# Performance work log

Hardware: AMD Instinct MI355X
Metric: run time of the kernel (lower is better)

Reference implementation:

```python
import jax, jax.numpy as jnp
import numpy as np

K = 8
B = 3.0
DIM = 32
HID = 32
BATCH = 65536
MIN_BW = 1e-3
MIN_BH = 1e-3
MIN_D = 1e-3


def setup_inputs() -> dict:
    key = jax.random.key(0)
    ks = jax.random.split(key, 8)
    L = DIM - 1
    x = jax.random.normal(ks[0], (BATCH, DIM), jnp.float32)
    init_param = jax.random.uniform(ks[1], (3 * K - 1,), jnp.float32, -0.5, 0.5)
    # stacked per-dim FCNN weights; layer l conditions on x[:, :l+1] -> causal zero-mask
    w1 = jax.random.normal(ks[2], (L, L, HID), jnp.float32) * 0.2
    mask = (jnp.arange(L)[None, :] <= jnp.arange(L)[:, None]).astype(jnp.float32)
    w1 = w1 * mask[:, :, None]
    b1 = jax.random.normal(ks[3], (L, HID), jnp.float32) * 0.1
    w2 = jax.random.normal(ks[4], (L, HID, HID), jnp.float32) * 0.2
    b2 = jax.random.normal(ks[5], (L, HID), jnp.float32) * 0.1
    w3 = jax.random.normal(ks[6], (L, HID, 3 * K - 1), jnp.float32) * 0.2
    b3 = jax.random.normal(ks[7], (L, 3 * K - 1), jnp.float32) * 0.1
    return {"x": x, "init_param": init_param, "w1": w1, "b1": b1,
            "w2": w2, "b2": b2, "w3": w3, "b3": b3}


def _rqs_forward(x, Wu, Hu, Du):
    # x: [dim, batch]; Wu, Hu: [dim, batch, K]; Du: [dim, batch, K-1]
    inside = (x >= -B) & (x <= B)
    xc = jnp.clip(x, -B, B)
    # bin widths
    widths = jax.nn.softmax(Wu, axis=-1)
    widths = MIN_BW + (1.0 - MIN_BW * K) * widths
    cw = jnp.cumsum(widths, axis=-1)
    cw = jnp.concatenate([jnp.zeros(cw.shape[:-1] + (1,), cw.dtype), cw], axis=-1)
    cw = 2.0 * B * cw - B
    cw = cw.at[..., 0].set(-B).at[..., -1].set(B)
    widths = cw[..., 1:] - cw[..., :-1]
    # bin heights
    heights = jax.nn.softmax(Hu, axis=-1)
    heights = MIN_BH + (1.0 - MIN_BH * K) * heights
    ch = jnp.cumsum(heights, axis=-1)
    ch = jnp.concatenate([jnp.zeros(ch.shape[:-1] + (1,), ch.dtype), ch], axis=-1)
    ch = 2.0 * B * ch - B
    ch = ch.at[..., 0].set(-B).at[..., -1].set(B)
    heights = ch[..., 1:] - ch[..., :-1]
    # knot derivatives, edges pinned so softplus(const)+min_d = 1
    const = float(np.log(np.exp(1.0 - MIN_D) - 1.0))
    pad = jnp.full(Du.shape[:-1] + (1,), const, Du.dtype)
    derivs = MIN_D + jax.nn.softplus(jnp.concatenate([pad, Du, pad], axis=-1))  # [.., K+1]
    # bin search (searchsorted on cumwidths, eps bump on last edge)
    cw_s = cw.at[..., -1].add(1e-6)
    idx = jnp.sum((xc[..., None] >= cw_s).astype(jnp.int32), axis=-1) - 1
    idx = jnp.clip(idx, 0, K - 1)
    g = lambda a: jnp.take_along_axis(a, idx[..., None], axis=-1)[..., 0]
    in_cw = g(cw)
    in_w = g(widths)
    in_ch = g(ch)
    in_h = g(heights)
    in_delta = g(heights / widths)
    d0 = g(derivs)
    d1 = g(derivs[..., 1:])
    theta = (xc - in_cw) / in_w
    tt = theta * (1.0 - theta)
    num = in_h * (in_delta * theta ** 2 + d0 * tt)
    den = in_delta + (d0 + d1 - 2.0 * in_delta) * tt
    out = in_ch + num / den
    dnum = in_delta ** 2 * (d1 * theta ** 2 + 2.0 * in_delta * tt + d0 * (1.0 - theta) ** 2)
    ld = jnp.log(dnum) - 2.0 * jnp.log(den)
    out = jnp.where(inside, out, x)  # identity tails
    ld = jnp.where(inside, ld, 0.0)
    return out, ld


def reference(x, init_param, w1, b1, w2, b2, w3, b3):
    # all per-dim conditioners at once (w1 is causally masked in setup)
    h1 = jnp.tanh(jnp.einsum('bd,ldh->lbh', x[:, :DIM - 1], w1) + b1[:, None, :])
    h2 = jnp.tanh(jnp.einsum('lbh,lhg->lbg', h1, w2) + b2[:, None, :])
    out = jnp.einsum('lbh,lho->lbo', h2, w3) + b3[:, None, :]  # [dim-1, batch, 3K-1]
    p0 = jnp.broadcast_to(init_param, (1, x.shape[0], 3 * K - 1))
    params = jnp.concatenate([p0, out], axis=0)  # [dim, batch, 3K-1]
    Wu = 2.0 * B * jax.nn.softmax(params[..., :K], axis=-1)
    Hu = 2.0 * B * jax.nn.softmax(params[..., K:2 * K], axis=-1)
    Du = jax.nn.softplus(params[..., 2 * K:])
    z_t, ld = _rqs_forward(x.T, Wu, Hu, Du)  # [dim, batch]
    return z_t.T, jnp.sum(ld, axis=0)
```

## Files before the change

kernel.cpp:

```cpp
#include <hip/hip_runtime.h>
#include <hip/hip_bf16.h>
#include <cmath>

constexpr int KN   = 8;
constexpr int NPAR = 23;
constexpr int DD   = 32;
constexpr float BND   = 3.0f;
constexpr float MINBW = 1e-3f;
constexpr float MIND  = 1e-3f;

#define TPB   64
#define ROWS  64
#define GDIMS 4
#define WST   40
#define PSTH  28
#define RECB  8192

typedef __attribute__((ext_vector_type(8))) short short8;
typedef __attribute__((ext_vector_type(4))) float float4v;
typedef __attribute__((ext_vector_type(2))) __fp16 fp16x2;
typedef __attribute__((ext_vector_type(4))) _Float16 half4v;

#define RCP(x) __builtin_amdgcn_rcpf(x)

#if __has_builtin(__builtin_amdgcn_exp2f)
#define EXP2(x) __builtin_amdgcn_exp2f(x)
#else
#define EXP2(x) __expf((x) * 0.6931471805599453f)
#endif
#if __has_builtin(__builtin_amdgcn_logf)
#define LOG2F(x) __builtin_amdgcn_logf(x)
#else
#define LOG2F(x) __log2f(x)
#endif
#define MED3(x, lo, hi) __builtin_amdgcn_fmed3f((x), (lo), (hi))

constexpr float L2E = 1.4426950408889634f;
constexpr float LN2 = 0.6931471805599453f;

__device__ __forceinline__ short f2bf(float f) {
    unsigned u = __float_as_uint(f);
    u += 0x7fffu + ((u >> 16) & 1u);
    return (short)(u >> 16);
}

__device__ __forceinline__ int pkbf(float a, float b) {
    union { __hip_bfloat162 v; int i; } u;
    u.v = __float22bfloat162_rn(make_float2(a, b));
    return u.i;
}

__device__ __forceinline__ int pkh(float a, float b) {
    union { fp16x2 h; int i; } u;
    u.h = __builtin_amdgcn_cvt_pkrtz(a, b);
    return u.i;
}

__device__ __forceinline__ float4v tanh4v(float4v c) {
    constexpr float C2L = 2.0f * L2E;
    float e0 = EXP2(MED3(c[0], -10.f, 10.f) * C2L);
    float e1 = EXP2(MED3(c[1], -10.f, 10.f) * C2L);
    float e2 = EXP2(MED3(c[2], -10.f, 10.f) * C2L);
    float e3 = EXP2(MED3(c[3], -10.f, 10.f) * C2L);
    float a0 = e0 + 1.f, a1 = e1 + 1.f, a2 = e2 + 1.f, a3 = e3 + 1.f;
    float p01 = a0 * a1, p23 = a2 * a3;
    float r   = RCP(p01 * p23);
    float r01 = r * p23;
    float r23 = r * p01;
    float4v o;
    o[0] = fmaf(-2.f, r01 * a1, 1.f);
    o[1] = fmaf(-2.f, r01 * a0, 1.f);
    o[2] = fmaf(-2.f, r23 * a3, 1.f);
    o[3] = fmaf(-2.f, r23 * a2, 1.f);
    return o;
}

__device__ __forceinline__ float rqs_apply(float xv, const float* p, float& ldout) {
    constexpr float C1 = 2.0f * BND * MINBW;
    constexpr float FC = 2.0f * BND * (1.0f - MINBW * KN);

    float t0w[KN], t0h[KN];
#pragma unroll
    for (int k = 0; k < KN; ++k) t0w[k] = EXP2(p[k]);
#pragma unroll
    for (int k = 0; k < KN; ++k) t0h[k] = EXP2(p[KN + k]);
    float sw = ((t0w[0] + t0w[1]) + (t0w[2] + t0w[3]))
             + ((t0w[4] + t0w[5]) + (t0w[6] + t0w[7]));
    float sh = ((t0h[0] + t0h[1]) + (t0h[2] + t0h[3]))
             + ((t0h[4] + t0h[5]) + (t0h[6] + t0h[7]));
    float r1   = RCP(sw * sh);
    float invw = (2.0f * BND * L2E) * (r1 * sh);
    float invh = (2.0f * BND * L2E) * (r1 * sw);
    float e2w[KN], e2h[KN];
#pragma unroll
    for (int k = 0; k < KN; ++k) e2w[k] = EXP2(t0w[k] * invw);
#pragma unroll
    for (int k = 0; k < KN; ++k) e2h[k] = EXP2(t0h[k] * invh);
    float s2w = ((e2w[0] + e2w[1]) + (e2w[2] + e2w[3]))
              + ((e2w[4] + e2w[5]) + (e2w[6] + e2w[7]));
    float s2h = ((e2h[0] + e2h[1]) + (e2h[2] + e2h[3]))
              + ((e2h[4] + e2h[5]) + (e2h[6] + e2h[7]));
    float r2   = RCP(s2w * s2h);
    float facw = FC * (r2 * s2h);
    float fach = FC * (r2 * s2w);

    float xc = MED3(xv, -BND, BND);

    float w0 = fmaf(facw, e2w[0], C1);
    float h0 = fmaf(fach, e2h[0], C1);
    float in_cw = -BND, in_w = w0, in_ch = -BND, in_h = h0;
    float dl0 = 0.0f, dl1 = p[2 * KN];
    bool e0 = true, e1 = false;
    float cwk = -BND + w0;
    float chk = -BND + h0;
#pragma unroll
    for (int k = 1; k < KN; ++k) {
        float wk = fmaf(facw, e2w[k], C1);
        float hk = fmaf(fach, e2h[k], C1);
        bool c = (xc >= cwk);
        in_cw = c ? cwk : in_cw;
        in_w  = c ? wk  : in_w;
        in_ch = c ? chk : in_ch;
        in_h  = c ? hk  : in_h;
        dl0   = c ? p[2 * KN + k - 1] : dl0;
        if (k < KN - 1) dl1 = c ? p[2 * KN + k] : dl1;
        if (k == 1)      e0 = !c;
        if (k == KN - 1) e1 = c;
        cwk += wk;
        chk += hk;
    }
    in_w = e1 ? (BND - in_cw) : in_w;
    in_h = e1 ? (BND - in_ch) : in_h;

    float sp0 = LOG2F(2.0f + EXP2(dl0));
    float sp1 = LOG2F(2.0f + EXP2(dl1));
    float d0 = e0 ? 1.0f : fmaf(LN2, sp0, MIND);
    float d1 = e1 ? 1.0f : fmaf(LN2, sp1, MIND);

    float u  = xc - in_cw;
    float v  = in_w - u;
    float s  = in_w, h = in_h;
    float uu = u * u, vv = v * v, uv = u * v;
    float uvs = uv * s;
    float t   = fmaf(v, v, uu);
    float dd  = d0 + d1;
    float DEN = fmaf(h, t, dd * uvs);
    float rD  = RCP(DEN);
    float NUM = fmaf(h, uu, d0 * uvs);
    float z   = fmaf(h * NUM, rD, in_ch);
    float t2  = fmaf(d0, vv, d1 * uu);
    float DN  = fmaf(h + h, uv, t2 * s);
    float h2s = (h * h) * s;
    float larg = ((h2s * DN) * rD) * rD;

    bool inside = (xv >= -BND) && (xv <= BND);
    ldout = inside ? LN2 * LOG2F(larg) : 0.0f;
    return inside ? z : xv;
}

__device__ __forceinline__ short8 xpose_h(float4v cA, float4v cB,
                                          int odd, int sl_a, int sl_b, bool qlow) {
    float4v tA = tanh4v(cA);
    float4v tB = tanh4v(cB);
    int a0 = pkbf(tA[0], tA[1]);
    int a1 = pkbf(tA[2], tA[3]);
    int b0 = pkbf(tB[0], tB[1]);
    int b1 = pkbf(tB[2], tB[3]);
    int p0 = odd ? b0 : a0, p1 = odd ? b1 : a1;
    int p2 = odd ? a0 : b0, p3 = odd ? a1 : b1;
    int g0 = __shfl(p0, sl_a, 64);
    int g1 = __shfl(p1, sl_a, 64);
    int g2 = __shfl(p2, sl_b, 64);
    int g3 = __shfl(p3, sl_b, 64);
    union { int4 i; short8 s; } u;
    u.i = qlow ? make_int4(g0, g1, g2, g3) : make_int4(g2, g3, g0, g1);
    return u.s;
}

__device__ __forceinline__ float4v f4v(float4 v) {
    float4v r; r[0] = v.x; r[1] = v.y; r[2] = v.z; r[3] = v.w; return r;
}

struct WFrag {
    short8 w1a, w1b, w2a, w2b, w3a, w3b;
    float4v bA1, bB1, bA2, bB2, bA3, bB3;
};

__device__ __forceinline__ WFrag load_wfrag(const char* __restrict__ wbuf,
                                            int l, int ln, int q) {
    const char* rec = wbuf + (size_t)l * RECB;
    const short* rw = (const short*)rec;
    const float* rb = (const float*)(rec + 7680);
    WFrag f;
    f.w1a = *(const short8*)&rw[ln * WST + q * 8];
    f.w1b = *(const short8*)&rw[(16 + ln) * WST + q * 8];
    f.w2a = *(const short8*)&rw[1280 + ln * WST + q * 8];
    f.w2b = *(const short8*)&rw[1280 + (16 + ln) * WST + q * 8];
    f.w3a = *(const short8*)&rw[2560 + ln * WST + q * 8];
    f.w3b = *(const short8*)&rw[2560 + (16 + ln) * WST + q * 8];
    f.bA1 = f4v(*(const float4*)&rb[4 * q]);
    f.bB1 = f4v(*(const float4*)&rb[16 + 4 * q]);
    f.bA2 = f4v(*(const float4*)&rb[32 + 4 * q]);
    f.bB2 = f4v(*(const float4*)&rb[48 + 4 * q]);
    f.bA3 = f4v(*(const float4*)&rb[64 + 4 * q]);
    f.bB3 = f4v(*(const float4*)&rb[80 + 4 * q]);
    return f;
}

extern "C" __global__ void __launch_bounds__(256)
k_prep(const float* __restrict__ w1, const float* __restrict__ b1,
       const float* __restrict__ w2, const float* __restrict__ b2,
       const float* __restrict__ w3, const float* __restrict__ b3,
       char* __restrict__ wbuf, float* __restrict__ ldo, int B)
{
    const int l = blockIdx.x, tid = threadIdx.x;
    if (l >= 31) {
        const int zb = l - 31;
        const int chunk = B >> 6;
        float4* dst = (float4*)(ldo + (size_t)zb * chunk);
        for (int i = tid; i < (chunk >> 2); i += 256)
            dst[i] = make_float4(0.f, 0.f, 0.f, 0.f);
        return;
    }
    short* r1 = (short*)(wbuf + (size_t)l * RECB);
    short* r2 = r1 + 1280;
    short* r3 = r2 + 1280;
    float* f1 = (float*)(wbuf + (size_t)l * RECB + 7680);
    float* f2 = f1 + 32;
    float* f3 = f2 + 32;
    const float* g1 = w1 + (size_t)l * 992;
    const float* g2 = w2 + (size_t)l * 1024;
    const float* g3 = w3 + (size_t)l * 736;
    for (int i = tid; i < 1280; i += 256) {
        int n = i / WST, k = i - WST * n;
        r1[i] = (k < 31) ? f2bf(g1[k * 32 + n]) : (short)0;
        r2[i] = (k < 32) ? f2bf(g2[k * 32 + n]) : (short)0;
        r3[i] = (n < 23 && k < 32) ? f2bf(g3[k * 23 + n] * L2E) : (short)0;
    }
    if (tid < 32) { f1[tid] = b1[(size_t)l * 32 + tid]; f2[tid] = b2[(size_t)l * 32 + tid]; }
    if (tid < 32) f3[tid] = (tid < 23) ? b3[(size_t)l * 23 + tid] * L2E : 0.0f;
}

extern "C" __global__ void __launch_bounds__(TPB, 2)
k_nsf(const float* __restrict__ x,
      const float* __restrict__ p0,
      const char* __restrict__ wbuf,
      float* __restrict__ zo, float* __restrict__ ldo, int B)
{
    __shared__ __align__(16) _Float16 sP[ROWS * PSTH];

    const int tid  = threadIdx.x;
    const int lane = tid & 63;
    const int q    = lane >> 4;
    const int ln   = lane & 15;
    const int qb   = q & 1;
    const bool qlow = (q < 2);
    const int s_even = ln + 32 * qb;
    const int s_odd  = s_even + 16;
    const int sl_a = qlow ? s_even : s_odd;
    const int sl_b = qlow ? s_odd  : s_even;
    const int g    = blockIdx.y;
    const int ly0  = GDIMS * g;
    const long long rowbase = (long long)blockIdx.x * ROWS;
    const long long row = rowbase + tid;

    float xarr[GDIMS];
    {
        float4 xs = *(const float4*)(x + row * DD + ly0);
        xarr[0] = xs.x; xarr[1] = xs.y; xarr[2] = xs.z; xarr[3] = xs.w;
    }

    short8 au[4];
#pragma unroll
    for (int t = 0; t < 4; ++t) {
        const int m0 = 16 * t;
        const float4* xp = (const float4*)(x + (rowbase + m0 + ln) * DD + q * 8);
        float4 uu = xp[0], vv = xp[1];
        union { int4 i; short8 s; } c;
        c.i = make_int4(pkbf(uu.x, uu.y), pkbf(uu.z, uu.w),
                        pkbf(vv.x, vv.y), pkbf(vv.z, vv.w));
        au[t] = c.s;
    }

    float zreg[GDIMS];
    float ldacc = 0.0f;

    WFrag wf = load_wfrag(wbuf, (ly0 == 0) ? 0 : ly0 - 1, ln, q);

#pragma unroll
    for (int j = 0; j < GDIMS; ++j) {
        const int ly = ly0 + j;
        if (ly == 0) {
            float pr[NPAR];
#pragma unroll
            for (int k = 0; k < NPAR; ++k) pr[k] = p0[k] * L2E;
            float ld;
            zreg[0] = rqs_apply(xarr[0], pr, ld);
            ldacc += ld;
            continue;
        }

        float4v cA[4], cB[4];
#pragma unroll
        for (int t = 0; t < 4; ++t) {
            cA[t] = __builtin_amdgcn_mfma_f32_16x16x32_bf16(wf.w1a, au[t], wf.bA1, 0, 0, 0);
            cB[t] = __builtin_amdgcn_mfma_f32_16x16x32_bf16(wf.w1b, au[t], wf.bB1, 0, 0, 0);
        }
        short8 h1f[4];
#pragma unroll
        for (int t = 0; t < 4; ++t)
            h1f[t] = xpose_h(cA[t], cB[t], qb, sl_a, sl_b, qlow);
#pragma unroll
        for (int t = 0; t < 4; ++t) {
            cA[t] = __builtin_amdgcn_mfma_f32_16x16x32_bf16(wf.w2a, h1f[t], wf.bA2, 0, 0, 0);
            cB[t] = __builtin_amdgcn_mfma_f32_16x16x32_bf16(wf.w2b, h1f[t], wf.bB2, 0, 0, 0);
        }
#pragma unroll
        for (int t = 0; t < 4; ++t)
            h1f[t] = xpose_h(cA[t], cB[t], qb, sl_a, sl_b, qlow);
#pragma unroll
        for (int t = 0; t < 4; ++t) {
            cA[t] = __builtin_amdgcn_mfma_f32_16x16x32_bf16(wf.w3a, h1f[t], wf.bA3, 0, 0, 0);
            cB[t] = __builtin_amdgcn_mfma_f32_16x16x32_bf16(wf.w3b, h1f[t], wf.bB3, 0, 0, 0);
        }
#pragma unroll
        for (int t = 0; t < 4; ++t) {
            const int m0 = 16 * t;
            int2 pv0 = make_int2(pkh(cA[t][0], cA[t][1]), pkh(cA[t][2], cA[t][3]));
            *(int2*)&sP[(m0 + ln) * PSTH + 4 * q] = pv0;
            if (qlow) {
                int2 pv1 = make_int2(pkh(cB[t][0], cB[t][1]), pkh(cB[t][2], cB[t][3]));
                *(int2*)&sP[(m0 + ln) * PSTH + 16 + 4 * q] = pv1;
            }
        }

        WFrag wfn;
        if (j + 1 < GDIMS) wfn = load_wfrag(wbuf, ly, ln, q);

        {
            const _Float16* pp = &sP[tid * PSTH];
            float pr[24];
#pragma unroll
            for (int u = 0; u < 6; ++u) {
                half4v hv = *(const half4v*)(pp + 4 * u);
                pr[4*u+0] = (float)hv[0];
                pr[4*u+1] = (float)hv[1];
                pr[4*u+2] = (float)hv[2];
                pr[4*u+3] = (float)hv[3];
            }
            float ld;
            zreg[j] = rqs_apply(xarr[j], pr, ld);
            ldacc += ld;
        }
        if (j + 1 < GDIMS) wf = wfn;
    }

    float4 zv = make_float4(zreg[0], zreg[1], zreg[2], zreg[3]);
    *(float4*)(zo + row * DD + ly0) = zv;
    unsafeAtomicAdd(&ldo[row], ldacc);
}

extern "C" void kernel_launch(void* const* d_in, const int* in_sizes, int n_in,
                              void* d_out, int out_size, void* d_ws, size_t ws_size,
                              hipStream_t stream) {
    const float* x  = (const float*)d_in[0];
    const float* p0 = (const float*)d_in[1];
    const float* w1 = (const float*)d_in[2];
    const float* b1 = (const float*)d_in[3];
    const float* w2 = (const float*)d_in[4];
    const float* b2 = (const float*)d_in[5];
    const float* w3 = (const float*)d_in[6];
    const float* b3 = (const float*)d_in[7];

    const int B = in_sizes[0] / DD;
    float* zo  = (float*)d_out;
    float* ldo = zo + (size_t)B * DD;
    char* wbuf = (char*)d_ws;

    hipLaunchKernelGGL(k_prep, dim3(95), dim3(256), 0, stream,
                       w1, b1, w2, b2, w3, b3, wbuf, ldo, B);
    hipLaunchKernelGGL(k_nsf, dim3(B / ROWS, DD / GDIMS), dim3(TPB), 0, stream,
                       x, p0, wbuf, zo, ldo, B);
}
```

Measured before the change: 136.3 us.

## Use Pade tanh, fp32 param staging in LDS, simplified shuffle transpose

```diff
diff --git a/kernel.cpp b/kernel.cpp
--- a/kernel.cpp
+++ b/kernel.cpp
@@ -13,13 +13,11 @@
 #define ROWS  64
 #define GDIMS 4
 #define WST   40
-#define PSTH  28
+#define PSTF  28
 #define RECB  8192
 
 typedef __attribute__((ext_vector_type(8))) short short8;
 typedef __attribute__((ext_vector_type(4))) float float4v;
-typedef __attribute__((ext_vector_type(2))) __fp16 fp16x2;
-typedef __attribute__((ext_vector_type(4))) _Float16 half4v;
 
 #define RCP(x) __builtin_amdgcn_rcpf(x)
 
@@ -50,28 +48,37 @@
     return u.i;
 }
 
-__device__ __forceinline__ int pkh(float a, float b) {
-    union { fp16x2 h; int i; } u;
-    u.h = __builtin_amdgcn_cvt_pkrtz(a, b);
-    return u.i;
-}
-
 __device__ __forceinline__ float4v tanh4v(float4v c) {
-    constexpr float C2L = 2.0f * L2E;
-    float e0 = EXP2(MED3(c[0], -10.f, 10.f) * C2L);
-    float e1 = EXP2(MED3(c[1], -10.f, 10.f) * C2L);
-    float e2 = EXP2(MED3(c[2], -10.f, 10.f) * C2L);
-    float e3 = EXP2(MED3(c[3], -10.f, 10.f) * C2L);
-    float a0 = e0 + 1.f, a1 = e1 + 1.f, a2 = e2 + 1.f, a3 = e3 + 1.f;
-    float p01 = a0 * a1, p23 = a2 * a3;
+    float n0, n1, n2, n3, d0, d1, d2, d3;
+    {
+        float x = MED3(c[0], -4.f, 4.f), x2 = x * x;
+        n0 = x * fmaf(x2, x2 + 105.f, 945.f);
+        d0 = fmaf(x2, fmaf(15.f, x2, 420.f), 945.f);
+    }
+    {
+        float x = MED3(c[1], -4.f, 4.f), x2 = x * x;
+        n1 = x * fmaf(x2, x2 + 105.f, 945.f);
+        d1 = fmaf(x2, fmaf(15.f, x2, 420.f), 945.f);
+    }
+    {
+        float x = MED3(c[2], -4.f, 4.f), x2 = x * x;
+        n2 = x * fmaf(x2, x2 + 105.f, 945.f);
+        d2 = fmaf(x2, fmaf(15.f, x2, 420.f), 945.f);
+    }
+    {
+        float x = MED3(c[3], -4.f, 4.f), x2 = x * x;
+        n3 = x * fmaf(x2, x2 + 105.f, 945.f);
+        d3 = fmaf(x2, fmaf(15.f, x2, 420.f), 945.f);
+    }
+    float p01 = d0 * d1, p23 = d2 * d3;
     float r   = RCP(p01 * p23);
     float r01 = r * p23;
     float r23 = r * p01;
     float4v o;
-    o[0] = fmaf(-2.f, r01 * a1, 1.f);
-    o[1] = fmaf(-2.f, r01 * a0, 1.f);
-    o[2] = fmaf(-2.f, r23 * a3, 1.f);
-    o[3] = fmaf(-2.f, r23 * a2, 1.f);
+    o[0] = n0 * (r01 * d1);
+    o[1] = n1 * (r01 * d0);
+    o[2] = n2 * (r23 * d3);
+    o[3] = n3 * (r23 * d2);
     return o;
 }
 
@@ -159,21 +166,23 @@
 }
 
 __device__ __forceinline__ short8 xpose_h(float4v cA, float4v cB,
-                                          int odd, int sl_a, int sl_b, bool qlow) {
+                                          int sl_a, int sl_b, bool qlow) {
     float4v tA = tanh4v(cA);
     float4v tB = tanh4v(cB);
     int a0 = pkbf(tA[0], tA[1]);
     int a1 = pkbf(tA[2], tA[3]);
     int b0 = pkbf(tB[0], tB[1]);
     int b1 = pkbf(tB[2], tB[3]);
-    int p0 = odd ? b0 : a0, p1 = odd ? b1 : a1;
-    int p2 = odd ? a0 : b0, p3 = odd ? a1 : b1;
-    int g0 = __shfl(p0, sl_a, 64);
-    int g1 = __shfl(p1, sl_a, 64);
-    int g2 = __shfl(p2, sl_b, 64);
-    int g3 = __shfl(p3, sl_b, 64);
+    int gA0 = __shfl(a0, sl_a, 64);
+    int gA1 = __shfl(a1, sl_a, 64);
+    int gA2 = __shfl(a0, sl_b, 64);
+    int gA3 = __shfl(a1, sl_b, 64);
+    int gB0 = __shfl(b0, sl_a, 64);
+    int gB1 = __shfl(b1, sl_a, 64);
+    int gB2 = __shfl(b0, sl_b, 64);
+    int gB3 = __shfl(b1, sl_b, 64);
     union { int4 i; short8 s; } u;
-    u.i = qlow ? make_int4(g0, g1, g2, g3) : make_int4(g2, g3, g0, g1);
+    u.i = qlow ? make_int4(gA0, gA1, gA2, gA3) : make_int4(gB0, gB1, gB2, gB3);
     return u.s;
 }
 
@@ -247,7 +256,7 @@
       const char* __restrict__ wbuf,
       float* __restrict__ zo, float* __restrict__ ldo, int B)
 {
-    __shared__ __align__(16) _Float16 sP[ROWS * PSTH];
+    __shared__ __align__(16) float sPf[ROWS * PSTF];
 
     const int tid  = threadIdx.x;
     const int lane = tid & 63;
@@ -255,10 +264,8 @@
     const int ln   = lane & 15;
     const int qb   = q & 1;
     const bool qlow = (q < 2);
-    const int s_even = ln + 32 * qb;
-    const int s_odd  = s_even + 16;
-    const int sl_a = qlow ? s_even : s_odd;
-    const int sl_b = qlow ? s_odd  : s_even;
+    const int sl_a = ln + 32 * qb;
+    const int sl_b = sl_a + 16;
     const int g    = blockIdx.y;
     const int ly0  = GDIMS * g;
     const long long rowbase = (long long)blockIdx.x * ROWS;
@@ -309,7 +316,7 @@
         short8 h1f[4];
 #pragma unroll
         for (int t = 0; t < 4; ++t)
-            h1f[t] = xpose_h(cA[t], cB[t], qb, sl_a, sl_b, qlow);
+            h1f[t] = xpose_h(cA[t], cB[t], sl_a, sl_b, qlow);
 #pragma unroll
         for (int t = 0; t < 4; ++t) {
             cA[t] = __builtin_amdgcn_mfma_f32_16x16x32_bf16(wf.w2a, h1f[t], wf.bA2, 0, 0, 0);
@@ -317,7 +324,7 @@
         }
 #pragma unroll
         for (int t = 0; t < 4; ++t)
-            h1f[t] = xpose_h(cA[t], cB[t], qb, sl_a, sl_b, qlow);
+            h1f[t] = xpose_h(cA[t], cB[t], sl_a, sl_b, qlow);
 #pragma unroll
         for (int t = 0; t < 4; ++t) {
             cA[t] = __builtin_amdgcn_mfma_f32_16x16x32_bf16(wf.w3a, h1f[t], wf.bA3, 0, 0, 0);
@@ -326,27 +333,24 @@
 #pragma unroll
         for (int t = 0; t < 4; ++t) {
             const int m0 = 16 * t;
-            int2 pv0 = make_int2(pkh(cA[t][0], cA[t][1]), pkh(cA[t][2], cA[t][3]));
-            *(int2*)&sP[(m0 + ln) * PSTH + 4 * q] = pv0;
-            if (qlow) {
-                int2 pv1 = make_int2(pkh(cB[t][0], cB[t][1]), pkh(cB[t][2], cB[t][3]));
-                *(int2*)&sP[(m0 + ln) * PSTH + 16 + 4 * q] = pv1;
-            }
+            *(float4v*)&sPf[(m0 + ln) * PSTF + 4 * q] = cA[t];
+            if (qlow)
+                *(float4v*)&sPf[(m0 + ln) * PSTF + 16 + 4 * q] = cB[t];
         }
 
         WFrag wfn;
         if (j + 1 < GDIMS) wfn = load_wfrag(wbuf, ly, ln, q);
 
         {
-            const _Float16* pp = &sP[tid * PSTH];
+            const float* pp = &sPf[tid * PSTF];
             float pr[24];
 #pragma unroll
             for (int u = 0; u < 6; ++u) {
-                half4v hv = *(const half4v*)(pp + 4 * u);
-                pr[4*u+0] = (float)hv[0];
-                pr[4*u+1] = (float)hv[1];
-                pr[4*u+2] = (float)hv[2];
-                pr[4*u+3] = (float)hv[3];
+                float4v hv = *(const float4v*)(pp + 4 * u);
+                pr[4*u+0] = hv[0];
+                pr[4*u+1] = hv[1];
+                pr[4*u+2] = hv[2];
+                pr[4*u+3] = hv[3];
             }
             float ld;
             zreg[j] = rqs_apply(xarr[j], pr, ld);
```

Measured after the change: 144.5 us. 6.0% more time.
